# Kernel optimization log

Hardware: AMD Instinct MI355X
Metric: run time of the kernel (lower is better)

The kernel has to match this reference:

```python
import jax, jax.numpy as jnp
import numpy as np
from jax import lax

NUM_OBJECTS = 3
KERNEL_DIM = 3
REDUCTION = 8


def setup_inputs() -> dict:
    key = jax.random.key(0)
    k1, k2, k3 = jax.random.split(key, 3)
    bs, C, h, w = 8, 256, 64, 64
    steps = 3
    f_e = jax.random.normal(k1, (bs, C, h, w), dtype=jnp.float32)
    # [steps, num_objects*k*k, bs, emb_dim]
    all_prototypes = jax.random.normal(k2, (steps, NUM_OBJECTS * KERNEL_DIM * KERNEL_DIM, bs, C), dtype=jnp.float32) * 0.05
    w_head = jax.random.normal(k3, (C,), dtype=jnp.float32) * 0.05
    b_head = jnp.zeros((1,), dtype=jnp.float32)
    return {"f_e": f_e, "all_prototypes": all_prototypes, "w_head": w_head, "b_head": b_head}


def reference(f_e, all_prototypes, w_head, b_head):
    bs, C, h, w = f_e.shape
    steps = all_prototypes.shape[0]
    no, k = NUM_OBJECTS, KERNEL_DIM
    pad = k // 2
    # tile f_e over objects -> single-batch multi-channel input, [1, bs*no*C, h, w]
    lhs = jnp.broadcast_to(f_e[:, None], (bs, no, C, h, w)).reshape(1, bs * no * C, h, w)
    groups = bs * no * C
    outs = []
    for i in range(steps):  # small fixed loop over iterative OPE steps
        # [no*k*k, bs, C] -> [bs, no, C, k, k]
        protos = (all_prototypes[i]
                  .transpose(1, 0, 2)
                  .reshape(bs, no, k, k, C)
                  .transpose(0, 1, 4, 2, 3))
        rhs = protos.reshape(groups, 1, k, k)
        # depthwise correlation, groups = bs*no*C (matches F.conv2d with groups)
        resp = lax.conv_general_dilated(
            lhs, rhs, window_strides=(1, 1), padding=[(pad, pad), (pad, pad)],
            feature_group_count=groups,
            dimension_numbers=("NCHW", "OIHW", "NCHW"),
        ).reshape(bs, no, C, h, w)
        # softmax over object axis, then softmax-weighted sum over objects
        sm = jax.nn.softmax(resp, axis=1)
        reduced = jnp.sum(sm * resp, axis=1)  # [bs, C, h, w]
        dmap = jax.nn.relu(jnp.einsum("bchw,c->bhw", reduced, w_head) + b_head[0])[:, None]
        up = jax.image.resize(dmap, (bs, 1, h * REDUCTION, w * REDUCTION), method="bilinear")
        outs.append(up)
    return jnp.stack(outs)  # [steps, bs, 1, H, W]; outs[-1] is final, rest aux
```

## Files before the change

### kernel.cpp

```cpp
#include <hip/hip_runtime.h>
#include <math.h>

#define STEPS 3
#define BS 8
#define NCH 256
#define H 64
#define W 64
#define UP 8
#define OH (H*UP)
#define OW (W*UP)
#define GB 16
#define CPB (NCH/GB)
#define CPW (CPB/4)
#define WREC 32
#define DMAP_FLOATS (STEPS*BS*H*W)
#define PREP_N (STEPS*28*BS*NCH)

__global__ __launch_bounds__(256) void loca_prep(
    const float* __restrict__ ap, const float* __restrict__ w_head,
    float* __restrict__ wt)
{
    int t = blockIdx.x * 256 + threadIdx.x;
    if (t >= PREP_N) return;
    int c = t & (NCH - 1);
    int r = t >> 8;
    int b = r & (BS - 1);
    r >>= 3;
    int j = r % 28;
    int i = r / 28;
    float v = (j < 27) ? ap[(((size_t)i * 27 + j) * BS + b) * NCH + c] : w_head[c];
    wt[(((size_t)b * NCH + c) * STEPS + i) * WREC + j] = v;
}

__global__ __launch_bounds__(256) void loca_dmap(
    const float* __restrict__ f_e,
    const float* __restrict__ wt,
    float* __restrict__ partial)
{
    __shared__ float wlds[CPB * STEPS * WREC];
    __shared__ float red[4][STEPS][256];

    const int tid  = threadIdx.x;
    const int lane = tid & 63;
    const int wv   = tid >> 6;
    const int rb   = blockIdx.x;
    const int b    = blockIdx.y;
    const int g    = blockIdx.z;
    const int row  = rb * 4 + (lane >> 4);
    const int xg   = lane & 15;
    const int C0   = g * CPB;

    {
        const float4* src = (const float4*)(wt + ((size_t)b * NCH + C0) * (STEPS * WREC));
        float4* dst = (float4*)wlds;
        dst[tid] = src[tid];
        if (tid < CPB * STEPS * WREC / 4 - 256)
            dst[256 + tid] = src[256 + tid];
    }
    __syncthreads();

    const float m_m1 = (row > 0)     ? 1.f : 0.f;
    const float m_p1 = (row < H - 1) ? 1.f : 0.f;
    const int r_m1 = row > 0     ? row - 1 : 0;
    const int r_p1 = row < H - 1 ? row + 1 : H - 1;

    const int cw = C0 + wv * CPW;
    const float* fb = f_e + ((size_t)b * NCH + cw) * (H * W);

    float acc[STEPS][4] = {};

    float4 nm = ((const float4*)(fb + r_m1 * W))[xg];
    float4 n0 = ((const float4*)(fb + row  * W))[xg];
    float4 np = ((const float4*)(fb + r_p1 * W))[xg];

    for (int cc = 0; cc < CPW; ++cc) {
        float4 vm = nm, v0 = n0, vp = np;
        if (cc + 1 < CPW) {
            const float* fc = fb + (cc + 1) * (H * W);
            nm = ((const float4*)(fc + r_m1 * W))[xg];
            n0 = ((const float4*)(fc + row  * W))[xg];
            np = ((const float4*)(fc + r_p1 * W))[xg];
        }
        vm.x *= m_m1; vm.y *= m_m1; vm.z *= m_m1; vm.w *= m_m1;
        vp.x *= m_p1; vp.y *= m_p1; vp.z *= m_p1; vp.w *= m_p1;

        float Lm = __shfl_up(vm.w, 1);
        float L0 = __shfl_up(v0.w, 1);
        float Lp = __shfl_up(vp.w, 1);
        float Rm = __shfl_down(vm.x, 1);
        float R0 = __shfl_down(v0.x, 1);
        float Rp = __shfl_down(vp.x, 1);
        if (xg == 0)  { Lm = 0.f; L0 = 0.f; Lp = 0.f; }
        if (xg == 15) { Rm = 0.f; R0 = 0.f; Rp = 0.f; }

        float am[6]  = {Lm, vm.x, vm.y, vm.z, vm.w, Rm};
        float a0[6]  = {L0, v0.x, v0.y, v0.z, v0.w, R0};
        float apv[6] = {Lp, vp.x, vp.y, vp.z, vp.w, Rp};

        const int lc = wv * CPW + cc;

        #pragma unroll
        for (int i = 0; i < STEPS; ++i) {
            union { float4 v4[7]; float f[28]; } qq;
            const float4* wp4 = (const float4*)(wlds + ((size_t)lc * STEPS + i) * WREC);
            #pragma unroll
            for (int q = 0; q < 7; ++q) qq.v4[q] = wp4[q];
            const float wh = qq.f[27];

            #pragma unroll
            for (int k = 0; k < 4; ++k) {
                float r_[3];
                #pragma unroll
                for (int o = 0; o < 3; ++o) {
                    float t = am[k] * qq.f[o * 9 + 0];
                    t = fmaf(am[k+1],  qq.f[o * 9 + 1], t);
                    t = fmaf(am[k+2],  qq.f[o * 9 + 2], t);
                    t = fmaf(a0[k],    qq.f[o * 9 + 3], t);
                    t = fmaf(a0[k+1],  qq.f[o * 9 + 4], t);
                    t = fmaf(a0[k+2],  qq.f[o * 9 + 5], t);
                    t = fmaf(apv[k],   qq.f[o * 9 + 6], t);
                    t = fmaf(apv[k+1], qq.f[o * 9 + 7], t);
                    t = fmaf(apv[k+2], qq.f[o * 9 + 8], t);
                    r_[o] = t;
                }
                float mx = fmaxf(r_[0], fmaxf(r_[1], r_[2]));
                float e0 = __expf(r_[0] - mx);
                float e1 = __expf(r_[1] - mx);
                float e2 = __expf(r_[2] - mx);
                float num = fmaf(e0, r_[0], fmaf(e1, r_[1], e2 * r_[2]));
                float den = e0 + e1 + e2;
#if __has_builtin(__builtin_amdgcn_rcpf)
                float redv = num * __builtin_amdgcn_rcpf(den);
#else
                float redv = num / den;
#endif
                acc[i][k] = fmaf(wh, redv, acc[i][k]);
            }
        }
    }

    const int px = (lane >> 4) * 64 + xg * 4;
    #pragma unroll
    for (int i = 0; i < STEPS; ++i) {
        float4 a; a.x = acc[i][0]; a.y = acc[i][1]; a.z = acc[i][2]; a.w = acc[i][3];
        *(float4*)&red[wv][i][px] = a;
    }
    __syncthreads();
    #pragma unroll
    for (int i = 0; i < STEPS; ++i) {
        float4 s0 = *(const float4*)&red[0][i][px];
        float4 s1 = *(const float4*)&red[1][i][px];
        float4 s2 = *(const float4*)&red[2][i][px];
        float4 s3 = *(const float4*)&red[3][i][px];
        float4 s;
        s.x = (s0.x + s1.x) + (s2.x + s3.x);
        s.y = (s0.y + s1.y) + (s2.y + s3.y);
        s.z = (s0.z + s1.z) + (s2.z + s3.z);
        s.w = (s0.w + s1.w) + (s2.w + s3.w);
        *(float4*)&partial[(size_t)g * DMAP_FLOATS + ((size_t)(i * BS + b)) * (H * W)
                           + row * W + xg * 4] = s;
    }
}

__global__ __launch_bounds__(256) void loca_reduce(
    const float* __restrict__ partial, const float* __restrict__ b_head,
    float* __restrict__ dmap)
{
    const int t = blockIdx.x * 256 + threadIdx.x;
    const float4* p = (const float4*)partial;
    float4 s = p[t];
    #pragma unroll
    for (int g = 1; g < GB; ++g) {
        float4 q = p[(size_t)g * (DMAP_FLOATS / 4) + t];
        s.x += q.x; s.y += q.y; s.z += q.z; s.w += q.w;
    }
    const float bias = b_head[0];
    s.x = fmaxf(s.x + bias, 0.f);
    s.y = fmaxf(s.y + bias, 0.f);
    s.z = fmaxf(s.z + bias, 0.f);
    s.w = fmaxf(s.w + bias, 0.f);
    ((float4*)dmap)[t] = s;
}

__global__ __launch_bounds__(256) void loca_upsample(
    const float* __restrict__ dmap, float* __restrict__ out)
{
    const int idx  = blockIdx.x * 256 + threadIdx.x;
    const int gx   = idx & (OW / 4 - 1);
    const int rest = idx >> 7;
    const int Y    = rest & (OH - 1);
    const int ib   = rest >> 9;

    const float* d = dmap + (size_t)ib * H * W;

    float yin = (Y + 0.5f) * 0.125f - 0.5f;
    float fy0 = floorf(yin);
    int   iy  = (int)fy0;
    float fy  = yin - fy0;
    int y0c = min(max(iy, 0), H - 1);
    int y1c = min(max(iy + 1, 0), H - 1);
    const float* row0 = d + y0c * W;
    const float* row1 = d + y1c * W;

    float4 o;
    float* op = &o.x;
    #pragma unroll
    for (int j = 0; j < 4; ++j) {
        int X = gx * 4 + j;
        float xin = (X + 0.5f) * 0.125f - 0.5f;
        float fx0 = floorf(xin);
        int   ix  = (int)fx0;
        float fx  = xin - fx0;
        int x0c = min(max(ix, 0), W - 1);
        int x1c = min(max(ix + 1, 0), W - 1);
        float a00 = row0[x0c], a01 = row0[x1c];
        float a10 = row1[x0c], a11 = row1[x1c];
        float v0 = a00 + fx * (a01 - a00);
        float v1 = a10 + fx * (a11 - a10);
        op[j] = v0 + fy * (v1 - v0);
    }
    ((float4*)out)[idx] = o;
}

extern "C" void kernel_launch(void* const* d_in, const int* in_sizes, int n_in,
                              void* d_out, int out_size, void* d_ws, size_t ws_size,
                              hipStream_t stream) {
    const float* f_e    = (const float*)d_in[0];
    const float* ap     = (const float*)d_in[1];
    const float* w_head = (const float*)d_in[2];
    const float* b_head = (const float*)d_in[3];
    float* out  = (float*)d_out;
    float* dmap = (float*)d_ws;
    float* wt   = dmap + DMAP_FLOATS;
    float* partial = out;

    loca_prep<<<(PREP_N + 255) / 256, 256, 0, stream>>>(ap, w_head, wt);

    dim3 g1(16, BS, GB);
    loca_dmap<<<g1, 256, 0, stream>>>(f_e, wt, partial);

    loca_reduce<<<DMAP_FLOATS / 4 / 256, 256, 0, stream>>>(partial, b_head, dmap);

    const int groups = STEPS * BS * OH * OW / 4;
    loca_upsample<<<groups / 256, 256, 0, stream>>>(dmap, out);
}
```

Before: 120.0 us.

## Fuse partial reduction into upsample and read prototype weights directly from global

Removes the separate reduce kernel: each upsample block sums the 16 channel-group partials for the three input rows it needs, applies bias and ReLU into shared memory, then interpolates two output rows. Partials move to the workspace instead of aliasing the output buffer. The dmap kernel also drops its LDS staging of weights and barrier, loading wave-uniform weights straight from global, which may become scalar loads. Neighbouring blocks redundantly re-sum overlapping input rows, and the weight loads may add latency in the inner loop.

```diff
diff --git a/kernel.cpp b/kernel.cpp
--- a/kernel.cpp
+++ b/kernel.cpp
@@ -14,6 +14,7 @@
 #define CPW (CPB/4)
 #define WREC 32
 #define DMAP_FLOATS (STEPS*BS*H*W)
+#define WT_FLOATS (BS*NCH*STEPS*WREC)
 #define PREP_N (STEPS*28*BS*NCH)
 
 __global__ __launch_bounds__(256) void loca_prep(
@@ -37,7 +38,6 @@
     const float* __restrict__ wt,
     float* __restrict__ partial)
 {
-    __shared__ float wlds[CPB * STEPS * WREC];
     __shared__ float red[4][STEPS][256];
 
     const int tid  = threadIdx.x;
@@ -48,24 +48,15 @@
     const int g    = blockIdx.z;
     const int row  = rb * 4 + (lane >> 4);
     const int xg   = lane & 15;
-    const int C0   = g * CPB;
-
-    {
-        const float4* src = (const float4*)(wt + ((size_t)b * NCH + C0) * (STEPS * WREC));
-        float4* dst = (float4*)wlds;
-        dst[tid] = src[tid];
-        if (tid < CPB * STEPS * WREC / 4 - 256)
-            dst[256 + tid] = src[256 + tid];
-    }
-    __syncthreads();
+    const int cw   = g * CPB + wv * CPW;
 
     const float m_m1 = (row > 0)     ? 1.f : 0.f;
     const float m_p1 = (row < H - 1) ? 1.f : 0.f;
     const int r_m1 = row > 0     ? row - 1 : 0;
     const int r_p1 = row < H - 1 ? row + 1 : H - 1;
 
-    const int cw = C0 + wv * CPW;
     const float* fb = f_e + ((size_t)b * NCH + cw) * (H * W);
+    const float* wb = wt  + ((size_t)b * NCH + cw) * (STEPS * WREC);
 
     float acc[STEPS][4] = {};
 
@@ -97,30 +88,27 @@
         float a0[6]  = {L0, v0.x, v0.y, v0.z, v0.w, R0};
         float apv[6] = {Lp, vp.x, vp.y, vp.z, vp.w, Rp};
 
-        const int lc = wv * CPW + cc;
+        const float* wc = wb + cc * (STEPS * WREC);
 
         #pragma unroll
         for (int i = 0; i < STEPS; ++i) {
-            union { float4 v4[7]; float f[28]; } qq;
-            const float4* wp4 = (const float4*)(wlds + ((size_t)lc * STEPS + i) * WREC);
-            #pragma unroll
-            for (int q = 0; q < 7; ++q) qq.v4[q] = wp4[q];
-            const float wh = qq.f[27];
-
+            const float* w = wc + i * WREC;
+            const float wh = w[27];
             #pragma unroll
             for (int k = 0; k < 4; ++k) {
                 float r_[3];
                 #pragma unroll
                 for (int o = 0; o < 3; ++o) {
-                    float t = am[k] * qq.f[o * 9 + 0];
-                    t = fmaf(am[k+1],  qq.f[o * 9 + 1], t);
-                    t = fmaf(am[k+2],  qq.f[o * 9 + 2], t);
-                    t = fmaf(a0[k],    qq.f[o * 9 + 3], t);
-                    t = fmaf(a0[k+1],  qq.f[o * 9 + 4], t);
-                    t = fmaf(a0[k+2],  qq.f[o * 9 + 5], t);
-                    t = fmaf(apv[k],   qq.f[o * 9 + 6], t);
-                    t = fmaf(apv[k+1], qq.f[o * 9 + 7], t);
-                    t = fmaf(apv[k+2], qq.f[o * 9 + 8], t);
+                    const float* q = w + o * 9;
+                    float t = am[k] * q[0];
+                    t = fmaf(am[k+1],  q[1], t);
+                    t = fmaf(am[k+2],  q[2], t);
+                    t = fmaf(a0[k],    q[3], t);
+                    t = fmaf(a0[k+1],  q[4], t);
+                    t = fmaf(a0[k+2],  q[5], t);
+                    t = fmaf(apv[k],   q[6], t);
+                    t = fmaf(apv[k+1], q[7], t);
+                    t = fmaf(apv[k+2], q[8], t);
                     r_[o] = t;
                 }
                 float mx = fmaxf(r_[0], fmaxf(r_[1], r_[2]));
@@ -162,45 +150,43 @@
     }
 }
 
-__global__ __launch_bounds__(256) void loca_reduce(
+__global__ __launch_bounds__(256) void loca_upsample(
     const float* __restrict__ partial, const float* __restrict__ b_head,
-    float* __restrict__ dmap)
+    float* __restrict__ out)
 {
-    const int t = blockIdx.x * 256 + threadIdx.x;
-    const float4* p = (const float4*)partial;
-    float4 s = p[t];
-    #pragma unroll
-    for (int g = 1; g < GB; ++g) {
-        float4 q = p[(size_t)g * (DMAP_FLOATS / 4) + t];
-        s.x += q.x; s.y += q.y; s.z += q.z; s.w += q.w;
-    }
-    const float bias = b_head[0];
-    s.x = fmaxf(s.x + bias, 0.f);
-    s.y = fmaxf(s.y + bias, 0.f);
-    s.z = fmaxf(s.z + bias, 0.f);
-    s.w = fmaxf(s.w + bias, 0.f);
-    ((float4*)dmap)[t] = s;
-}
-
-__global__ __launch_bounds__(256) void loca_upsample(
-    const float* __restrict__ dmap, float* __restrict__ out)
-{
-    const int idx  = blockIdx.x * 256 + threadIdx.x;
-    const int gx   = idx & (OW / 4 - 1);
-    const int rest = idx >> 7;
-    const int Y    = rest & (OH - 1);
-    const int ib   = rest >> 9;
-
-    const float* d = dmap + (size_t)ib * H * W;
+    __shared__ float rows[3][W];
+
+    const int t  = threadIdx.x;
+    const int yp = blockIdx.x;
+    const int ib = blockIdx.y;
+    const int Y0 = yp * 2;
+
+    const float yin0 = (Y0 + 0.5f) * 0.125f - 0.5f;
+    const int   ry   = (int)floorf(yin0);
+
+    if (t < 3 * W) {
+        int r   = t >> 6;
+        int col = t & 63;
+        int rr  = min(max(ry + r, 0), H - 1);
+        const float* p = partial + (size_t)ib * (H * W) + rr * W + col;
+        float s = 0.f;
+        #pragma unroll
+        for (int g = 0; g < GB; ++g)
+            s += p[(size_t)g * DMAP_FLOATS];
+        rows[r][col] = fmaxf(s + b_head[0], 0.f);
+    }
+    __syncthreads();
+
+    const int lY = t >> 7;
+    const int gx = t & 127;
+    const int Y  = Y0 + lY;
 
     float yin = (Y + 0.5f) * 0.125f - 0.5f;
     float fy0 = floorf(yin);
     int   iy  = (int)fy0;
     float fy  = yin - fy0;
-    int y0c = min(max(iy, 0), H - 1);
-    int y1c = min(max(iy + 1, 0), H - 1);
-    const float* row0 = d + y0c * W;
-    const float* row1 = d + y1c * W;
+    const float* row0 = rows[iy - ry];
+    const float* row1 = rows[iy - ry + 1];
 
     float4 o;
     float* op = &o.x;
@@ -219,7 +205,7 @@
         float v1 = a10 + fx * (a11 - a10);
         op[j] = v0 + fy * (v1 - v0);
     }
-    ((float4*)out)[idx] = o;
+    ((float4*)out)[((size_t)ib * OH + Y) * (OW / 4) + gx] = o;
 }
 
 extern "C" void kernel_launch(void* const* d_in, const int* in_sizes, int n_in,
@@ -229,18 +215,15 @@
     const float* ap     = (const float*)d_in[1];
     const float* w_head = (const float*)d_in[2];
     const float* b_head = (const float*)d_in[3];
-    float* out  = (float*)d_out;
-    float* dmap = (float*)d_ws;
-    float* wt   = dmap + DMAP_FLOATS;
-    float* partial = out;
+    float* out     = (float*)d_out;
+    float* wt      = (float*)d_ws;
+    float* partial = wt + WT_FLOATS;
 
     loca_prep<<<(PREP_N + 255) / 256, 256, 0, stream>>>(ap, w_head, wt);
 
     dim3 g1(16, BS, GB);
     loca_dmap<<<g1, 256, 0, stream>>>(f_e, wt, partial);
 
-    loca_reduce<<<DMAP_FLOATS / 4 / 256, 256, 0, stream>>>(partial, b_head, dmap);
-
-    const int groups = STEPS * BS * OH * OW / 4;
-    loca_upsample<<<groups / 256, 256, 0, stream>>>(dmap, out);
-}
+    dim3 g2(OH / 2, STEPS * BS);
+    loca_upsample<<<g2, 256, 0, stream>>>(partial, b_head, out);
+}
```

New measurement: 134.8 us. 1.12x slower.
